# Kernel optimization log

Hardware: AMD Instinct MI355X
Metric: run time of the kernel (lower is better)

The kernel has to match this reference:

```python
import jax, jax.numpy as jnp
import numpy as np

H = 1024   # hidden_dim
NH = 16    # num_heads
HD = H // NH  # head_dim = 64
B, S = 2, 2048
LN_EPS = 1e-5


def setup_inputs() -> dict:
    key = jax.random.key(0)
    ks = jax.random.split(key, 5)
    scale = 1.0 / np.sqrt(H)  # xavier-ish scale for stability
    return {
        "x": jax.random.normal(ks[0], (B, S, H), dtype=jnp.float32),
        "Wq": jax.random.normal(ks[1], (H, H), dtype=jnp.float32) * scale,
        "bq": jnp.zeros((H,), jnp.float32),
        "Wk": jax.random.normal(ks[2], (H, H), dtype=jnp.float32) * scale,
        "bk": jnp.zeros((H,), jnp.float32),
        "Wv": jax.random.normal(ks[3], (H, H), dtype=jnp.float32) * scale,
        "bv": jnp.zeros((H,), jnp.float32),
        "Wo": jax.random.normal(ks[4], (H, H), dtype=jnp.float32) * scale,
        "bo": jnp.zeros((H,), jnp.float32),
        "ln_gamma": jnp.ones((H,), jnp.float32),
        "ln_beta": jnp.zeros((H,), jnp.float32),
    }


def reference(x, Wq, bq, Wk, bk, Wv, bv, Wo, bo, ln_gamma, ln_beta):
    b, s, _ = x.shape
    # QKV projections, split heads: (b, nh, s, hd)
    def split_heads(t):
        return t.reshape(b, s, NH, HD).transpose(0, 2, 1, 3)
    Q = split_heads(x @ Wq + bq)
    K = split_heads(x @ Wk + bk)
    V = split_heads(x @ Wv + bv)
    # scaled dot-product with clamp (mask=None path)
    scores = jnp.einsum('bhqd,bhkd->bhqk', Q, K) / np.sqrt(HD).astype(np.float32)
    scores = jnp.clip(scores, -10000.0, 10000.0)
    attn = jax.nn.softmax(scores, axis=-1)
    # dropout is identity in eval mode
    ctx = jnp.einsum('bhqk,bhkd->bhqd', attn, V)
    ctx = ctx.transpose(0, 2, 1, 3).reshape(b, s, H)
    out = ctx @ Wo + bo
    # residual + LayerNorm
    y = out + x
    mu = jnp.mean(y, axis=-1, keepdims=True)
    var = jnp.mean(jnp.square(y - mu), axis=-1, keepdims=True)
    y = (y - mu) * jax.lax.rsqrt(var + LN_EPS)
    return y * ln_gamma + ln_beta
```

## Files before the change

kernel.cpp:

```cpp
#include <hip/hip_runtime.h>

typedef unsigned short u16;
typedef __attribute__((ext_vector_type(8))) short shortx8;
typedef __attribute__((ext_vector_type(4))) float floatx4;
typedef __attribute__((ext_vector_type(2))) float floatx2;
typedef __attribute__((ext_vector_type(2))) unsigned uintx2;
typedef __attribute__((ext_vector_type(4))) unsigned uintx4;

#define GLD16(gp, lp) __builtin_amdgcn_global_load_lds( \
    (__attribute__((address_space(1))) void*)(gp), \
    (__attribute__((address_space(3))) void*)(lp), 16, 0, 0)

#define BAR() __builtin_amdgcn_s_barrier()
#define LGKM0() do { asm volatile("s_waitcnt lgkmcnt(0)" ::: "memory"); \
                     __builtin_amdgcn_sched_barrier(0); } while (0)
#define VMCNT0() do { asm volatile("s_waitcnt vmcnt(0)" ::: "memory"); \
                      __builtin_amdgcn_sched_barrier(0); } while (0)

__device__ __forceinline__ u16 f2bf(float f) {
  union { float f; unsigned u; } v; v.f = f;
  unsigned r = v.u + 0x7FFFu + ((v.u >> 16) & 1u);
  return (u16)(r >> 16);
}

__device__ __forceinline__ unsigned pkbf(float a, float b) {
#if __has_builtin(__builtin_amdgcn_cvt_pk_bf16_f32)
  auto r = __builtin_amdgcn_cvt_pk_bf16_f32(a, b);
  return __builtin_bit_cast(unsigned, r);
#else
  union { float f; unsigned u; } x, y; x.f = a; y.f = b;
  return __builtin_amdgcn_perm(y.u + 0x8000u, x.u + 0x8000u, 0x07060302u);
#endif
}

__global__ __launch_bounds__(256) void prep_kernel(const float* __restrict__ x,
                                                   u16* __restrict__ xb,
                                                   const float* __restrict__ Wq,
                                                   const float* __restrict__ Wk,
                                                   const float* __restrict__ Wv,
                                                   const float* __restrict__ Wo,
                                                   u16* __restrict__ Wt) {
  __shared__ u16 tile[32][33];
  int bid = blockIdx.x;
  int tid = threadIdx.x;
  if (bid < 4096) {
    int i = bid * 256 + tid;
    float4 v = ((const float4*)x)[i];
    uintx2 o;
    o.x = pkbf(v.x, v.y);
    o.y = pkbf(v.z, v.w);
    ((uintx2*)xb)[i] = o;
  } else {
    int block = bid - 4096;
    int mat = block >> 10;
    int rem = block & 1023;
    const float* W = (mat == 0) ? Wq : (mat == 1) ? Wk : (mat == 2) ? Wv : Wo;
    u16* dst = Wt + (size_t)mat * 1024 * 1024;
    int n0 = (rem & 31) * 32, k0 = (rem >> 5) * 32;
    int tx = tid & 31, ty = tid >> 5;
    for (int i = 0; i < 4; ++i)
      tile[ty + i * 8][tx] = f2bf(W[(size_t)(k0 + ty + i * 8) * 1024 + n0 + tx]);
    __syncthreads();
    for (int i = 0; i < 4; ++i)
      dst[(size_t)(n0 + ty + i * 8) * 1024 + k0 + tx] = tile[tx][ty + i * 8];
  }
}

template <int MIB>
__device__ __forceinline__ void qkv_lda(const u16* Ah, int lrow, int lcol,
                                        shortx8 (&afr)[2][2]) {
#pragma unroll
  for (int j = 0; j < 2; ++j) {
    int rm = (MIB + j) * 16 + lcol;
#pragma unroll
    for (int kk = 0; kk < 2; ++kk)
      afr[j][kk] = *(const shortx8*)&Ah[rm * 64 + (((kk * 4 + lrow) ^ (rm & 7)) * 8)];
  }
}

template <int MIB>
__device__ __forceinline__ void qkv_mfma(floatx4 (&acc)[8][4],
                                         const shortx8 (&afr)[2][2],
                                         const shortx8 (&bfr)[4][2]) {
#pragma unroll
  for (int kk = 0; kk < 2; ++kk)
#pragma unroll
    for (int j = 0; j < 2; ++j)
#pragma unroll
      for (int ni = 0; ni < 4; ++ni)
        acc[MIB + j][ni] = __builtin_amdgcn_mfma_f32_16x16x32_bf16(
            afr[j][kk], bfr[ni][kk], acc[MIB + j][ni], 0, 0, 0);
}

__global__ __launch_bounds__(512, 2) void qkv_gemm(const u16* __restrict__ xb,
                                                   const u16* __restrict__ Wt,
                                                   const float* __restrict__ bq,
                                                   const float* __restrict__ bk,
                                                   const float* __restrict__ bv,
                                                   u16* __restrict__ Qh,
                                                   u16* __restrict__ Kh,
                                                   u16* __restrict__ Vth) {
  __shared__ u16 lds[65536];
  const int tid = threadIdx.x;
  const int wave = tid >> 6, lane = tid & 63;
  const int lrow = lane >> 4, lcol = lane & 15;
  const int wm = wave >> 2, wn = wave & 3;
  const int m0 = blockIdx.x * 256;
  const int nt = blockIdx.y;
  const int mat = nt >> 2;
  const int n0 = (nt & 3) * 256;
  const u16* Ag = xb;
  const u16* Bg = Wt + (size_t)mat * 1048576;

  const u16* sa[2][2];
  const u16* sb[2][2];
#pragma unroll
  for (int h = 0; h < 2; ++h)
#pragma unroll
    for (int l = 0; l < 2; ++l) {
      int g = (l * 8 + wave) * 64 + lane;
      int r = g >> 3, c = g & 7;
      int cc = (c ^ (r & 7)) * 8;
      sa[h][l] = Ag + (size_t)(m0 + h * 128 + r) * 1024 + cc;
      sb[h][l] = Bg + (size_t)(n0 + h * 128 + r) * 1024 + cc;
    }

  floatx4 acc[8][4];
#pragma unroll
  for (int mi = 0; mi < 8; ++mi)
#pragma unroll
    for (int ni = 0; ni < 4; ++ni)
      acc[mi][ni] = (floatx4){0.f, 0.f, 0.f, 0.f};

#pragma unroll
  for (int h = 0; h < 2; ++h)
#pragma unroll
    for (int l = 0; l < 2; ++l) {
      GLD16(sa[h][l], lds + h * 8192 + (l * 8 + wave) * 512);
      GLD16(sb[h][l], lds + 16384 + h * 8192 + (l * 8 + wave) * 512);
    }
  VMCNT0();
  BAR();

#pragma unroll 2
  for (int t = 0; t < 16; ++t) {
    const int rb = t & 1, wb = rb ^ 1;
    const u16* Ah = lds + rb * 32768 + wm * 8192;
    const u16* Bh = lds + rb * 32768 + 16384 + (wn >> 1) * 8192;
    u16* Aw = lds + wb * 32768;
    u16* Bw = lds + wb * 32768 + 16384;

    if (t < 15) {
      int k64 = (t + 1) * 64;
#pragma unroll
      for (int l = 0; l < 2; ++l) {
        GLD16(sa[0][l] + k64, Aw + (l * 8 + wave) * 512);
        GLD16(sa[1][l] + k64, Aw + 8192 + (l * 8 + wave) * 512);
      }
    }
    shortx8 bfr[4][2];
#pragma unroll
    for (int ni = 0; ni < 4; ++ni) {
      int rn = (wn & 1) * 64 + ni * 16 + lcol;
#pragma unroll
      for (int kk = 0; kk < 2; ++kk)
        bfr[ni][kk] = *(const shortx8*)&Bh[rn * 64 + (((kk * 4 + lrow) ^ (rn & 7)) * 8)];
    }
    {
      shortx8 afr[2][2];
      qkv_lda<0>(Ah, lrow, lcol, afr);
      BAR();
      LGKM0();
      __builtin_amdgcn_s_setprio(1);
      qkv_mfma<0>(acc, afr, bfr);
      __builtin_amdgcn_s_setprio(0);
      BAR();
    }
    if (t < 15) {
      int k64 = (t + 1) * 64;
#pragma unroll
      for (int l = 0; l < 2; ++l) {
        GLD16(sb[0][l] + k64, Bw + (l * 8 + wave) * 512);
        GLD16(sb[1][l] + k64, Bw + 8192 + (l * 8 + wave) * 512);
      }
    }
    {
      shortx8 afr[2][2];
      qkv_lda<2>(Ah, lrow, lcol, afr);
      BAR();
      LGKM0();
      __builtin_amdgcn_s_setprio(1);
      qkv_mfma<2>(acc, afr, bfr);
      __builtin_amdgcn_s_setprio(0);
      BAR();
    }
    {
      shortx8 afr[2][2];
      qkv_lda<4>(Ah, lrow, lcol, afr);
      BAR();
      LGKM0();
      __builtin_amdgcn_s_setprio(1);
      qkv_mfma<4>(acc, afr, bfr);
      __builtin_amdgcn_s_setprio(0);
      BAR();
    }
    {
      shortx8 afr[2][2];
      qkv_lda<6>(Ah, lrow, lcol, afr);
      BAR();
      LGKM0();
      __builtin_amdgcn_s_setprio(1);
      qkv_mfma<6>(acc, afr, bfr);
      __builtin_amdgcn_s_setprio(0);
      VMCNT0();
      BAR();
    }
  }

  const float* bias = (mat == 0) ? bq : (mat == 1) ? bk : bv;
  const float qscale = 0.18033688011f;

  if (mat < 2) {
    u16* dst = (mat == 0) ? Qh : Kh;
    float sc = (mat == 0) ? qscale : 1.0f;
#pragma unroll
    for (int mi = 0; mi < 8; ++mi) {
      int mb = wm * 128 + mi * 16 + lrow * 4;
#pragma unroll
      for (int ni = 0; ni < 4; ++ni) {
        int n = wn * 64 + ni * 16 + lcol;
        float bval = bias[n0 + n];
#pragma unroll
        for (int r = 0; r < 4; ++r) {
          int m = mb + r;
          lds[m * 256 + (((n >> 3) ^ (m & 31)) * 8) + (n & 7)] =
              f2bf((acc[mi][ni][r] + bval) * sc);
        }
      }
    }
    __syncthreads();
    int row = tid >> 1, half = tid & 1;
    int m = m0 + row;
    int bb = m >> 11, s = m & 2047;
#pragma unroll
    for (int i = 0; i < 16; ++i) {
      int cg = half * 16 + i;
      int pg = cg ^ (row & 31);
      shortx8 v = *(const shortx8*)&lds[row * 256 + pg * 8];
      int ng = n0 + cg * 8;
      int hh = ng >> 6, d = ng & 63;
      *(shortx8*)&dst[((size_t)(bb * 16 + hh) * 2048 + s) * 64 + d] = v;
    }
  } else {
#pragma unroll
    for (int mi = 0; mi < 8; ++mi) {
      int mbase = m0 + wm * 128 + mi * 16 + lrow * 4;
      int bb = mbase >> 11, s = mbase & 2047;
#pragma unroll
      for (int ni = 0; ni < 4; ++ni) {
        int n = n0 + wn * 64 + ni * 16 + lcol;
        float bval = bias[n];
        int hh = n >> 6, d = n & 63;
        uintx2 pk;
        pk.x = pkbf(acc[mi][ni][0] + bval, acc[mi][ni][1] + bval);
        pk.y = pkbf(acc[mi][ni][2] + bval, acc[mi][ni][3] + bval);
        *(uintx2*)&Vth[((size_t)(bb * 16 + hh) * 64 + d) * 2048 + s] = pk;
      }
    }
  }
}

__global__ __launch_bounds__(256) void out_gemm(const u16* __restrict__ ctx,
                                                const u16* __restrict__ Wot,
                                                const float* __restrict__ bo,
                                                float* __restrict__ aout) {
  __shared__ u16 As[128 * 64];
  __shared__ u16 Bs[64 * 64];
  int m0 = blockIdx.x * 128;
  int n0 = blockIdx.y * 64;
  const int tid = threadIdx.x;
  const int wave = tid >> 6, lane = tid & 63;
  const int lrow = lane >> 4, lcol = lane & 15;
  const int wm = wave >> 1, wn = wave & 1;

  floatx4 acc[4][2];
  for (int mi = 0; mi < 4; ++mi)
    for (int ni = 0; ni < 2; ++ni)
      acc[mi][ni] = (floatx4){0.f, 0.f, 0.f, 0.f};

  const u16* ap[4];
  const u16* bp[2];
  for (int l = 0; l < 4; ++l) {
    int g = (l * 4 + wave) * 64 + lane;
    int r = g >> 3, c = g & 7;
    ap[l] = ctx + (size_t)(m0 + r) * 1024 + (c ^ (r & 7)) * 8;
  }
  for (int l = 0; l < 2; ++l) {
    int g = (l * 4 + wave) * 64 + lane;
    int r = g >> 3, c = g & 7;
    bp[l] = Wot + (size_t)(n0 + r) * 1024 + (c ^ (r & 7)) * 8;
  }

  for (int k0 = 0; k0 < 1024; k0 += 64) {
    __syncthreads();
    for (int l = 0; l < 4; ++l) { GLD16(ap[l], As + (l * 4 + wave) * 512); ap[l] += 64; }
    for (int l = 0; l < 2; ++l) { GLD16(bp[l], Bs + (l * 4 + wave) * 512); bp[l] += 64; }
    __syncthreads();
    for (int kk = 0; kk < 2; ++kk) {
      shortx8 af[4], bf[2];
      for (int mi = 0; mi < 4; ++mi) {
        int row = wm * 64 + mi * 16 + lcol;
        int gr = (kk * 4 + lrow) ^ (row & 7);
        af[mi] = *(const shortx8*)&As[row * 64 + gr * 8];
      }
      for (int ni = 0; ni < 2; ++ni) {
        int row = wn * 32 + ni * 16 + lcol;
        int gr = (kk * 4 + lrow) ^ (row & 7);
        bf[ni] = *(const shortx8*)&Bs[row * 64 + gr * 8];
      }
      for (int mi = 0; mi < 4; ++mi)
        for (int ni = 0; ni < 2; ++ni)
          acc[mi][ni] = __builtin_amdgcn_mfma_f32_16x16x32_bf16(af[mi], bf[ni], acc[mi][ni], 0, 0, 0);
    }
  }

  for (int mi = 0; mi < 4; ++mi) {
    int mbase = m0 + wm * 64 + mi * 16 + lrow * 4;
    for (int ni = 0; ni < 2; ++ni) {
      int n = n0 + wn * 32 + ni * 16 + lcol;
      float bval = bo[n];
      for (int r = 0; r < 4; ++r)
        aout[(size_t)(mbase + r) * 1024 + n] = acc[mi][ni][r] + bval;
    }
  }
}

__global__ __launch_bounds__(512) void attn_kernel(const u16* __restrict__ Qh,
                                                   const u16* __restrict__ Kh,
                                                   const u16* __restrict__ Vth,
                                                   u16* __restrict__ ctx) {
  __shared__ u16 QPs[128 * 64];
  __shared__ u16 Ks[2][64 * 64];
  __shared__ u16 Vs[2][64 * 64];

  int bh = blockIdx.x;
  int b = bh >> 4, h = bh & 15;
  int q0 = blockIdx.y * 128;
  int tid = threadIdx.x;
  int wave = tid >> 6, lane = tid & 63;
  int lrow = lane >> 4, lcol = lane & 15;

  const u16* Qg = Qh + ((size_t)bh * 2048 + q0) * 64;
  for (int l = 0; l < 2; ++l) {
    int g = (l * 8 + wave) * 64 + lane;
    int r = g >> 3, c = g & 7;
    GLD16(Qg + r * 64 + ((c ^ (r & 7)) * 8), QPs + (l * 8 + wave) * 512);
  }

  const u16* Kbase = Kh + (size_t)bh * 2048 * 64;
  const u16* Vbase = Vth + (size_t)bh * 64 * 2048;

  int g = wave * 64 + lane;
  int gr = g >> 3, gc = g & 7;
  int cc = (gc ^ (gr & 7)) * 8;
  const u16* kp = Kbase + (size_t)gr * 64 + cc;

  const u16* vp = Vbase + (size_t)gr * 2048 + gc * 8;
  int hh = gc >> 2, ct = gc & 3;
  int ua = 4 * (ct & 1) + (ct >> 1);
  int chunkA = hh * 4 + (ua >> 1);
  int offA = gr * 128 + ((chunkA ^ (gr & 7)) * 16) + (ua & 1) * 8;
  int offB = gr * 128 + (((chunkA + 1) ^ (gr & 7)) * 16) + (ua & 1) * 8;

  {
    float4 vreg = *(const float4*)vp;
    vp += 64;
    GLD16(kp, (u16*)Ks + wave * 512);
    kp += 4096;
    char* vb = (char*)Vs;
    *(floatx2*)(vb + offA) = (floatx2){vreg.x, vreg.y};
    *(floatx2*)(vb + offB) = (floatx2){vreg.z, vreg.w};
  }
  __syncthreads();

  shortx8 qf[2];
  for (int kk = 0; kk < 2; ++kk) {
    int row = wave * 16 + lcol;
    int grr = (kk * 4 + lrow) ^ (row & 7);
    qf[kk] = *(const shortx8*)&QPs[row * 64 + grr * 8];
  }

  const short one_bf = (short)0x3F80;
  const shortx8 ones8 = {one_bf, one_bf, one_bf, one_bf, one_bf, one_bf, one_bf, one_bf};

  floatx4 o[4];
  floatx4 lacc = (floatx4){0.f, 0.f, 0.f, 0.f};
  for (int dt = 0; dt < 4; ++dt) o[dt] = (floatx4){0.f, 0.f, 0.f, 0.f};

  for (int i = 0; i < 32; ++i) {
    int cur = i & 1;
    float4 vreg;
    if (i < 31) {
      vreg = *(const float4*)vp;
      vp += 64;
      GLD16(kp, (u16*)Ks + (cur ^ 1) * 4096 + wave * 512);
      kp += 4096;
    }

    floatx4 sc[4];
    for (int kt = 0; kt < 4; ++kt)
      sc[kt] = (floatx4){0.f, 0.f, 0.f, 0.f};
    __builtin_amdgcn_s_setprio(1);
    for (int kk = 0; kk < 2; ++kk) {
      for (int kt = 0; kt < 4; ++kt) {
        int row = kt * 16 + lcol;
        int grr = (kk * 4 + lrow) ^ (row & 7);
        shortx8 kf = *(const shortx8*)&Ks[cur][row * 64 + grr * 8];
        sc[kt] = __builtin_amdgcn_mfma_f32_16x16x32_bf16(kf, qf[kk], sc[kt], 0, 0, 0);
      }
    }
    __builtin_amdgcn_s_setprio(0);

    float p[4][4];
    for (int kt = 0; kt < 4; ++kt)
      for (int r = 0; r < 4; ++r)
        p[kt][r] = __builtin_amdgcn_exp2f(sc[kt][r]);
    shortx8 pf[2];
    for (int kk = 0; kk < 2; ++kk) {
      uintx4 w;
      w.x = pkbf(p[2 * kk][0], p[2 * kk][1]);
      w.y = pkbf(p[2 * kk][2], p[2 * kk][3]);
      w.z = pkbf(p[2 * kk + 1][0], p[2 * kk + 1][1]);
      w.w = pkbf(p[2 * kk + 1][2], p[2 * kk + 1][3]);
      pf[kk] = __builtin_bit_cast(shortx8, w);
    }

    if (i < 31) {
      char* vb = (char*)Vs + (cur ^ 1) * 8192;
      *(floatx2*)(vb + offA) = (floatx2){vreg.x, vreg.y};
      *(floatx2*)(vb + offB) = (floatx2){vreg.z, vreg.w};
    }

    __builtin_amdgcn_s_setprio(1);
    for (int kk = 0; kk < 2; ++kk) {
      lacc = __builtin_amdgcn_mfma_f32_16x16x32_bf16(ones8, pf[kk], lacc, 0, 0, 0);
      for (int dt = 0; dt < 4; ++dt) {
        int row = dt * 16 + lcol;
        int grr = (kk * 4 + lrow) ^ (row & 7);
        shortx8 vf = *(const shortx8*)&Vs[cur][row * 64 + grr * 8];
        o[dt] = __builtin_amdgcn_mfma_f32_16x16x32_bf16(vf, pf[kk], o[dt], 0, 0, 0);
      }
    }
    __builtin_amdgcn_s_setprio(0);
    __syncthreads();
  }

  {
    float inv = 1.0f / lacc[0];
    int s = q0 + wave * 16 + lcol;
    u16* dst = ctx + (size_t)(b * 2048 + s) * 1024 + h * 64 + lrow * 4;
    for (int dt = 0; dt < 4; ++dt) {
      uintx2 pk;
      pk.x = pkbf(o[dt][0] * inv, o[dt][1] * inv);
      pk.y = pkbf(o[dt][2] * inv, o[dt][3] * inv);
      *(uintx2*)(dst + dt * 16) = pk;
    }
  }
}

__global__ __launch_bounds__(256) void ln_kernel(const float* __restrict__ aout,
                                                 const float* __restrict__ x,
                                                 const float* __restrict__ gamma,
                                                 const float* __restrict__ beta,
                                                 float* __restrict__ out) {
  int row = blockIdx.x;
  int t = threadIdx.x;
  const float4* a4 = (const float4*)(aout + (size_t)row * 1024);
  const float4* x4 = (const float4*)(x + (size_t)row * 1024);
  float4 v = a4[t];
  float4 xv = x4[t];
  v.x += xv.x; v.y += xv.y; v.z += xv.z; v.w += xv.w;
  float s = v.x + v.y + v.z + v.w;
  float s2 = v.x * v.x + v.y * v.y + v.z * v.z + v.w * v.w;
  for (int off = 1; off < 64; off <<= 1) {
    s += __shfl_xor(s, off, 64);
    s2 += __shfl_xor(s2, off, 64);
  }
  __shared__ float red[8];
  int wave = t >> 6, lane = t & 63;
  if (lane == 0) { red[wave] = s; red[4 + wave] = s2; }
  __syncthreads();
  s = red[0] + red[1] + red[2] + red[3];
  s2 = red[4] + red[5] + red[6] + red[7];
  float mu = s * (1.0f / 1024.0f);
  float var = s2 * (1.0f / 1024.0f) - mu * mu;
  float rstd = rsqrtf(var + 1e-5f);
  float4 g = ((const float4*)gamma)[t];
  float4 be = ((const float4*)beta)[t];
  float4 y;
  y.x = (v.x - mu) * rstd * g.x + be.x;
  y.y = (v.y - mu) * rstd * g.y + be.y;
  y.z = (v.z - mu) * rstd * g.z + be.z;
  y.w = (v.w - mu) * rstd * g.w + be.w;
  ((float4*)(out + (size_t)row * 1024))[t] = y;
}

extern "C" void kernel_launch(void* const* d_in, const int* in_sizes, int n_in,
                              void* d_out, int out_size, void* d_ws, size_t ws_size,
                              hipStream_t stream) {
  const float* x     = (const float*)d_in[0];
  const float* Wq    = (const float*)d_in[1];
  const float* bq    = (const float*)d_in[2];
  const float* Wk    = (const float*)d_in[3];
  const float* bk    = (const float*)d_in[4];
  const float* Wv    = (const float*)d_in[5];
  const float* bv    = (const float*)d_in[6];
  const float* Wo    = (const float*)d_in[7];
  const float* bo    = (const float*)d_in[8];
  const float* gamma = (const float*)d_in[9];
  const float* beta  = (const float*)d_in[10];
  float* out = (float*)d_out;

  char* ws = (char*)d_ws;
  u16* xb   = (u16*)(ws);
  u16* Wt   = (u16*)(ws + ((size_t)8 << 20));
  u16* Qh   = (u16*)(ws + ((size_t)16 << 20));
  u16* Kh   = (u16*)(ws + ((size_t)24 << 20));
  u16* Vth  = (u16*)(ws + ((size_t)32 << 20));
  u16* ctx  = (u16*)(ws + ((size_t)40 << 20));
  float* aout = (float*)(ws + ((size_t)48 << 20));

  prep_kernel<<<8192, 256, 0, stream>>>(x, xb, Wq, Wk, Wv, Wo, Wt);
  qkv_gemm<<<dim3(16, 12), 512, 0, stream>>>(xb, Wt, bq, bk, bv, Qh, Kh, Vth);
  attn_kernel<<<dim3(32, 16), 512, 0, stream>>>(Qh, Kh, Vth, ctx);
  out_gemm<<<dim3(32, 16), 256, 0, stream>>>(ctx, Wt + (size_t)3 * 1024 * 1024, bo, aout);
  ln_kernel<<<4096, 256, 0, stream>>>(aout, x, gamma, beta, out);
}
```

Baseline: 193.6 us.

## Halve attention block to 4 waves, each handling two query sub-tiles

The attention kernel now runs 256 threads (4 waves) per block instead of 8, and each wave processes 32 query rows as two 16-row sub-tiles. Every K and V fragment read from LDS is reused for two MFMAs, which halves LDS read traffic per unit of compute. Each thread issues two global loads per tile, and the launch bounds ask for two blocks per CU. The cost is higher register pressure from the doubled accumulators and fewer waves per block to hide latency.

```diff
diff --git a/kernel.cpp b/kernel.cpp
--- a/kernel.cpp
+++ b/kernel.cpp
@@ -335,10 +335,10 @@
   }
 }
 
-__global__ __launch_bounds__(512) void attn_kernel(const u16* __restrict__ Qh,
-                                                   const u16* __restrict__ Kh,
-                                                   const u16* __restrict__ Vth,
-                                                   u16* __restrict__ ctx) {
+__global__ __launch_bounds__(256, 2) void attn_kernel(const u16* __restrict__ Qh,
+                                                      const u16* __restrict__ Kh,
+                                                      const u16* __restrict__ Vth,
+                                                      u16* __restrict__ ctx) {
   __shared__ u16 QPs[128 * 64];
   __shared__ u16 Ks[2][64 * 64];
   __shared__ u16 Vs[2][64 * 64];
@@ -351,118 +351,157 @@
   int lrow = lane >> 4, lcol = lane & 15;
 
   const u16* Qg = Qh + ((size_t)bh * 2048 + q0) * 64;
-  for (int l = 0; l < 2; ++l) {
-    int g = (l * 8 + wave) * 64 + lane;
+#pragma unroll
+  for (int l = 0; l < 4; ++l) {
+    int g = (l * 4 + wave) * 64 + lane;
     int r = g >> 3, c = g & 7;
-    GLD16(Qg + r * 64 + ((c ^ (r & 7)) * 8), QPs + (l * 8 + wave) * 512);
+    GLD16(Qg + r * 64 + ((c ^ (r & 7)) * 8), QPs + (l * 4 + wave) * 512);
   }
 
   const u16* Kbase = Kh + (size_t)bh * 2048 * 64;
   const u16* Vbase = Vth + (size_t)bh * 64 * 2048;
 
-  int g = wave * 64 + lane;
-  int gr = g >> 3, gc = g & 7;
-  int cc = (gc ^ (gr & 7)) * 8;
-  const u16* kp = Kbase + (size_t)gr * 64 + cc;
-
-  const u16* vp = Vbase + (size_t)gr * 2048 + gc * 8;
-  int hh = gc >> 2, ct = gc & 3;
-  int ua = 4 * (ct & 1) + (ct >> 1);
-  int chunkA = hh * 4 + (ua >> 1);
-  int offA = gr * 128 + ((chunkA ^ (gr & 7)) * 16) + (ua & 1) * 8;
-  int offB = gr * 128 + (((chunkA + 1) ^ (gr & 7)) * 16) + (ua & 1) * 8;
+  const u16* kp[2];
+  const u16* vp[2];
+  int offA[2], offB[2];
+#pragma unroll
+  for (int l = 0; l < 2; ++l) {
+    int g = (l * 4 + wave) * 64 + lane;
+    int gr = g >> 3, gc = g & 7;
+    kp[l] = Kbase + (size_t)gr * 64 + ((gc ^ (gr & 7)) * 8);
+    vp[l] = Vbase + (size_t)gr * 2048 + gc * 8;
+    int hh = gc >> 2, ct = gc & 3;
+    int ua = 4 * (ct & 1) + (ct >> 1);
+    int chunkA = hh * 4 + (ua >> 1);
+    offA[l] = gr * 128 + ((chunkA ^ (gr & 7)) * 16) + (ua & 1) * 8;
+    offB[l] = gr * 128 + (((chunkA + 1) ^ (gr & 7)) * 16) + (ua & 1) * 8;
+  }
 
   {
-    float4 vreg = *(const float4*)vp;
-    vp += 64;
-    GLD16(kp, (u16*)Ks + wave * 512);
-    kp += 4096;
+    float4 v0 = *(const float4*)vp[0];
+    float4 v1 = *(const float4*)vp[1];
+    vp[0] += 64; vp[1] += 64;
+    GLD16(kp[0], (u16*)Ks + wave * 512);
+    GLD16(kp[1], (u16*)Ks + (4 + wave) * 512);
+    kp[0] += 4096; kp[1] += 4096;
     char* vb = (char*)Vs;
-    *(floatx2*)(vb + offA) = (floatx2){vreg.x, vreg.y};
-    *(floatx2*)(vb + offB) = (floatx2){vreg.z, vreg.w};
+    *(floatx2*)(vb + offA[0]) = (floatx2){v0.x, v0.y};
+    *(floatx2*)(vb + offB[0]) = (floatx2){v0.z, v0.w};
+    *(floatx2*)(vb + offA[1]) = (floatx2){v1.x, v1.y};
+    *(floatx2*)(vb + offB[1]) = (floatx2){v1.z, v1.w};
   }
   __syncthreads();
 
-  shortx8 qf[2];
-  for (int kk = 0; kk < 2; ++kk) {
-    int row = wave * 16 + lcol;
-    int grr = (kk * 4 + lrow) ^ (row & 7);
-    qf[kk] = *(const shortx8*)&QPs[row * 64 + grr * 8];
-  }
+  shortx8 qf[2][2];
+#pragma unroll
+  for (int s = 0; s < 2; ++s)
+#pragma unroll
+    for (int kk = 0; kk < 2; ++kk) {
+      int row = wave * 32 + s * 16 + lcol;
+      int grr = (kk * 4 + lrow) ^ (row & 7);
+      qf[s][kk] = *(const shortx8*)&QPs[row * 64 + grr * 8];
+    }
 
   const short one_bf = (short)0x3F80;
   const shortx8 ones8 = {one_bf, one_bf, one_bf, one_bf, one_bf, one_bf, one_bf, one_bf};
 
-  floatx4 o[4];
-  floatx4 lacc = (floatx4){0.f, 0.f, 0.f, 0.f};
-  for (int dt = 0; dt < 4; ++dt) o[dt] = (floatx4){0.f, 0.f, 0.f, 0.f};
+  floatx4 o[2][4];
+  floatx4 lacc[2];
+#pragma unroll
+  for (int s = 0; s < 2; ++s) {
+    lacc[s] = (floatx4){0.f, 0.f, 0.f, 0.f};
+#pragma unroll
+    for (int dt = 0; dt < 4; ++dt) o[s][dt] = (floatx4){0.f, 0.f, 0.f, 0.f};
+  }
 
   for (int i = 0; i < 32; ++i) {
     int cur = i & 1;
-    float4 vreg;
+    float4 v0, v1;
     if (i < 31) {
-      vreg = *(const float4*)vp;
-      vp += 64;
-      GLD16(kp, (u16*)Ks + (cur ^ 1) * 4096 + wave * 512);
-      kp += 4096;
-    }
-
-    floatx4 sc[4];
-    for (int kt = 0; kt < 4; ++kt)
-      sc[kt] = (floatx4){0.f, 0.f, 0.f, 0.f};
+      v0 = *(const float4*)vp[0];
+      v1 = *(const float4*)vp[1];
+      vp[0] += 64; vp[1] += 64;
+      GLD16(kp[0], (u16*)Ks + (cur ^ 1) * 4096 + wave * 512);
+      GLD16(kp[1], (u16*)Ks + (cur ^ 1) * 4096 + (4 + wave) * 512);
+      kp[0] += 4096; kp[1] += 4096;
+    }
+
+    floatx4 sc[2][4];
+#pragma unroll
+    for (int s = 0; s < 2; ++s)
+#pragma unroll
+      for (int kt = 0; kt < 4; ++kt)
+        sc[s][kt] = (floatx4){0.f, 0.f, 0.f, 0.f};
     __builtin_amdgcn_s_setprio(1);
+#pragma unroll
     for (int kk = 0; kk < 2; ++kk) {
+#pragma unroll
       for (int kt = 0; kt < 4; ++kt) {
         int row = kt * 16 + lcol;
         int grr = (kk * 4 + lrow) ^ (row & 7);
         shortx8 kf = *(const shortx8*)&Ks[cur][row * 64 + grr * 8];
-        sc[kt] = __builtin_amdgcn_mfma_f32_16x16x32_bf16(kf, qf[kk], sc[kt], 0, 0, 0);
+        sc[0][kt] = __builtin_amdgcn_mfma_f32_16x16x32_bf16(kf, qf[0][kk], sc[0][kt], 0, 0, 0);
+        sc[1][kt] = __builtin_amdgcn_mfma_f32_16x16x32_bf16(kf, qf[1][kk], sc[1][kt], 0, 0, 0);
       }
     }
     __builtin_amdgcn_s_setprio(0);
 
-    float p[4][4];
-    for (int kt = 0; kt < 4; ++kt)
-      for (int r = 0; r < 4; ++r)
-        p[kt][r] = __builtin_amdgcn_exp2f(sc[kt][r]);
-    shortx8 pf[2];
-    for (int kk = 0; kk < 2; ++kk) {
-      uintx4 w;
-      w.x = pkbf(p[2 * kk][0], p[2 * kk][1]);
-      w.y = pkbf(p[2 * kk][2], p[2 * kk][3]);
-      w.z = pkbf(p[2 * kk + 1][0], p[2 * kk + 1][1]);
-      w.w = pkbf(p[2 * kk + 1][2], p[2 * kk + 1][3]);
-      pf[kk] = __builtin_bit_cast(shortx8, w);
+    shortx8 pf[2][2];
+#pragma unroll
+    for (int s = 0; s < 2; ++s) {
+      float p[4][4];
+#pragma unroll
+      for (int kt = 0; kt < 4; ++kt)
+#pragma unroll
+        for (int r = 0; r < 4; ++r)
+          p[kt][r] = __builtin_amdgcn_exp2f(sc[s][kt][r]);
+#pragma unroll
+      for (int kk = 0; kk < 2; ++kk) {
+        uintx4 w;
+        w.x = pkbf(p[2 * kk][0], p[2 * kk][1]);
+        w.y = pkbf(p[2 * kk][2], p[2 * kk][3]);
+        w.z = pkbf(p[2 * kk + 1][0], p[2 * kk + 1][1]);
+        w.w = pkbf(p[2 * kk + 1][2], p[2 * kk + 1][3]);
+        pf[s][kk] = __builtin_bit_cast(shortx8, w);
+      }
     }
 
     if (i < 31) {
       char* vb = (char*)Vs + (cur ^ 1) * 8192;
-      *(floatx2*)(vb + offA) = (floatx2){vreg.x, vreg.y};
-      *(floatx2*)(vb + offB) = (floatx2){vreg.z, vreg.w};
+      *(floatx2*)(vb + offA[0]) = (floatx2){v0.x, v0.y};
+      *(floatx2*)(vb + offB[0]) = (floatx2){v0.z, v0.w};
+      *(floatx2*)(vb + offA[1]) = (floatx2){v1.x, v1.y};
+      *(floatx2*)(vb + offB[1]) = (floatx2){v1.z, v1.w};
     }
 
     __builtin_amdgcn_s_setprio(1);
+#pragma unroll
     for (int kk = 0; kk < 2; ++kk) {
-      lacc = __builtin_amdgcn_mfma_f32_16x16x32_bf16(ones8, pf[kk], lacc, 0, 0, 0);
+      lacc[0] = __builtin_amdgcn_mfma_f32_16x16x32_bf16(ones8, pf[0][kk], lacc[0], 0, 0, 0);
+      lacc[1] = __builtin_amdgcn_mfma_f32_16x16x32_bf16(ones8, pf[1][kk], lacc[1], 0, 0, 0);
+#pragma unroll
       for (int dt = 0; dt < 4; ++dt) {
         int row = dt * 16 + lcol;
         int grr = (kk * 4 + lrow) ^ (row & 7);
         shortx8 vf = *(const shortx8*)&Vs[cur][row * 64 + grr * 8];
-        o[dt] = __builtin_amdgcn_mfma_f32_16x16x32_bf16(vf, pf[kk], o[dt], 0, 0, 0);
+        o[0][dt] = __builtin_amdgcn_mfma_f32_16x16x32_bf16(vf, pf[0][kk], o[0][dt], 0, 0, 0);
+        o[1][dt] = __builtin_amdgcn_mfma_f32_16x16x32_bf16(vf, pf[1][kk], o[1][dt], 0, 0, 0);
       }
     }
     __builtin_amdgcn_s_setprio(0);
     __syncthreads();
   }
 
-  {
-    float inv = 1.0f / lacc[0];
-    int s = q0 + wave * 16 + lcol;
-    u16* dst = ctx + (size_t)(b * 2048 + s) * 1024 + h * 64 + lrow * 4;
+#pragma unroll
+  for (int s = 0; s < 2; ++s) {
+    float inv = 1.0f / lacc[s][0];
+    int sq = q0 + wave * 32 + s * 16 + lcol;
+    u16* dst = ctx + (size_t)(b * 2048 + sq) * 1024 + h * 64 + lrow * 4;
+#pragma unroll
     for (int dt = 0; dt < 4; ++dt) {
       uintx2 pk;
-      pk.x = pkbf(o[dt][0] * inv, o[dt][1] * inv);
-      pk.y = pkbf(o[dt][2] * inv, o[dt][3] * inv);
+      pk.x = pkbf(o[s][dt][0] * inv, o[s][dt][1] * inv);
+      pk.y = pkbf(o[s][dt][2] * inv, o[s][dt][3] * inv);
       *(uintx2*)(dst + dt * 16) = pk;
     }
   }
@@ -532,7 +571,7 @@
 
   prep_kernel<<<8192, 256, 0, stream>>>(x, xb, Wq, Wk, Wv, Wo, Wt);
   qkv_gemm<<<dim3(16, 12), 512, 0, stream>>>(xb, Wt, bq, bk, bv, Qh, Kh, Vth);
-  attn_kernel<<<dim3(32, 16), 512, 0, stream>>>(Qh, Kh, Vth, ctx);
+  attn_kernel<<<dim3(32, 16), 256, 0, stream>>>(Qh, Kh, Vth, ctx);
   out_gemm<<<dim3(32, 16), 256, 0, stream>>>(ctx, Wt + (size_t)3 * 1024 * 1024, bo, aout);
   ln_kernel<<<4096, 256, 0, stream>>>(aout, x, gamma, beta, out);
 }
```

New measurement: 199.0 us. 1.03x slower.

## Double-buffer LDS in output projection GEMM with split-phase prefetch

Applied to the files above, without the earlier changes.

Rewrites the out_gemm main loop to use two LDS buffers. The next k-tile's A and B loads are issued asynchronously while MFMAs run on the current tile, with the work split into two half-phases under barriers and raised wave priority around the MFMA bursts. The aim is to hide global-to-LDS load latency that the old load/sync/compute loop exposed. In exchange it doubles LDS use and adds more barriers and a launch_bounds occupancy hint.

```diff
diff --git a/kernel.cpp b/kernel.cpp
--- a/kernel.cpp
+++ b/kernel.cpp
@@ -270,65 +270,129 @@
   }
 }
 
-__global__ __launch_bounds__(256) void out_gemm(const u16* __restrict__ ctx,
-                                                const u16* __restrict__ Wot,
-                                                const float* __restrict__ bo,
-                                                float* __restrict__ aout) {
-  __shared__ u16 As[128 * 64];
-  __shared__ u16 Bs[64 * 64];
-  int m0 = blockIdx.x * 128;
-  int n0 = blockIdx.y * 64;
+__global__ __launch_bounds__(256, 2) void out_gemm(const u16* __restrict__ ctx,
+                                                   const u16* __restrict__ Wot,
+                                                   const float* __restrict__ bo,
+                                                   float* __restrict__ aout) {
+  __shared__ u16 lds[24576];
   const int tid = threadIdx.x;
   const int wave = tid >> 6, lane = tid & 63;
   const int lrow = lane >> 4, lcol = lane & 15;
   const int wm = wave >> 1, wn = wave & 1;
-
-  floatx4 acc[4][2];
-  for (int mi = 0; mi < 4; ++mi)
-    for (int ni = 0; ni < 2; ++ni)
-      acc[mi][ni] = (floatx4){0.f, 0.f, 0.f, 0.f};
-
-  const u16* ap[4];
-  const u16* bp[2];
+  const int m0 = blockIdx.x * 128;
+  const int n0 = blockIdx.y * 64;
+
+  const u16* sa[4];
+  const u16* sb[2];
+#pragma unroll
   for (int l = 0; l < 4; ++l) {
     int g = (l * 4 + wave) * 64 + lane;
     int r = g >> 3, c = g & 7;
-    ap[l] = ctx + (size_t)(m0 + r) * 1024 + (c ^ (r & 7)) * 8;
-  }
+    sa[l] = ctx + (size_t)(m0 + r) * 1024 + ((c ^ (r & 7)) * 8);
+  }
+#pragma unroll
   for (int l = 0; l < 2; ++l) {
     int g = (l * 4 + wave) * 64 + lane;
     int r = g >> 3, c = g & 7;
-    bp[l] = Wot + (size_t)(n0 + r) * 1024 + (c ^ (r & 7)) * 8;
-  }
-
-  for (int k0 = 0; k0 < 1024; k0 += 64) {
-    __syncthreads();
-    for (int l = 0; l < 4; ++l) { GLD16(ap[l], As + (l * 4 + wave) * 512); ap[l] += 64; }
-    for (int l = 0; l < 2; ++l) { GLD16(bp[l], Bs + (l * 4 + wave) * 512); bp[l] += 64; }
-    __syncthreads();
-    for (int kk = 0; kk < 2; ++kk) {
-      shortx8 af[4], bf[2];
-      for (int mi = 0; mi < 4; ++mi) {
-        int row = wm * 64 + mi * 16 + lcol;
-        int gr = (kk * 4 + lrow) ^ (row & 7);
-        af[mi] = *(const shortx8*)&As[row * 64 + gr * 8];
-      }
-      for (int ni = 0; ni < 2; ++ni) {
-        int row = wn * 32 + ni * 16 + lcol;
-        int gr = (kk * 4 + lrow) ^ (row & 7);
-        bf[ni] = *(const shortx8*)&Bs[row * 64 + gr * 8];
-      }
-      for (int mi = 0; mi < 4; ++mi)
-        for (int ni = 0; ni < 2; ++ni)
-          acc[mi][ni] = __builtin_amdgcn_mfma_f32_16x16x32_bf16(af[mi], bf[ni], acc[mi][ni], 0, 0, 0);
-    }
-  }
-
+    sb[l] = Wot + (size_t)(n0 + r) * 1024 + ((c ^ (r & 7)) * 8);
+  }
+
+  floatx4 acc[4][2];
+#pragma unroll
+  for (int mi = 0; mi < 4; ++mi)
+#pragma unroll
+    for (int ni = 0; ni < 2; ++ni)
+      acc[mi][ni] = (floatx4){0.f, 0.f, 0.f, 0.f};
+
+#pragma unroll
+  for (int l = 0; l < 4; ++l) GLD16(sa[l], lds + (l * 4 + wave) * 512);
+#pragma unroll
+  for (int l = 0; l < 2; ++l) GLD16(sb[l], lds + 8192 + (l * 4 + wave) * 512);
+  VMCNT0();
+  BAR();
+
+#pragma unroll 2
+  for (int t = 0; t < 16; ++t) {
+    const int rb = t & 1, wb = rb ^ 1;
+    const u16* Ab = lds + rb * 12288;
+    const u16* Bb = lds + rb * 12288 + 8192;
+    u16* Aw = lds + wb * 12288;
+    u16* Bw = lds + wb * 12288 + 8192;
+    const int k64 = (t + 1) * 64;
+
+    if (t < 15) {
+#pragma unroll
+      for (int l = 0; l < 4; ++l) GLD16(sa[l] + k64, Aw + (l * 4 + wave) * 512);
+    }
+    shortx8 bfr[2][2];
+#pragma unroll
+    for (int ni = 0; ni < 2; ++ni) {
+      int rn = wn * 32 + ni * 16 + lcol;
+#pragma unroll
+      for (int kk = 0; kk < 2; ++kk)
+        bfr[ni][kk] = *(const shortx8*)&Bb[rn * 64 + (((kk * 4 + lrow) ^ (rn & 7)) * 8)];
+    }
+    {
+      shortx8 afr[2][2];
+#pragma unroll
+      for (int j = 0; j < 2; ++j) {
+        int rm = wm * 64 + j * 16 + lcol;
+#pragma unroll
+        for (int kk = 0; kk < 2; ++kk)
+          afr[j][kk] = *(const shortx8*)&Ab[rm * 64 + (((kk * 4 + lrow) ^ (rm & 7)) * 8)];
+      }
+      BAR();
+      LGKM0();
+      __builtin_amdgcn_s_setprio(1);
+#pragma unroll
+      for (int kk = 0; kk < 2; ++kk)
+#pragma unroll
+        for (int j = 0; j < 2; ++j)
+#pragma unroll
+          for (int ni = 0; ni < 2; ++ni)
+            acc[j][ni] = __builtin_amdgcn_mfma_f32_16x16x32_bf16(
+                afr[j][kk], bfr[ni][kk], acc[j][ni], 0, 0, 0);
+      __builtin_amdgcn_s_setprio(0);
+      BAR();
+    }
+    if (t < 15) {
+#pragma unroll
+      for (int l = 0; l < 2; ++l) GLD16(sb[l] + k64, Bw + (l * 4 + wave) * 512);
+    }
+    {
+      shortx8 afr[2][2];
+#pragma unroll
+      for (int j = 0; j < 2; ++j) {
+        int rm = wm * 64 + (2 + j) * 16 + lcol;
+#pragma unroll
+        for (int kk = 0; kk < 2; ++kk)
+          afr[j][kk] = *(const shortx8*)&Ab[rm * 64 + (((kk * 4 + lrow) ^ (rm & 7)) * 8)];
+      }
+      BAR();
+      LGKM0();
+      __builtin_amdgcn_s_setprio(1);
+#pragma unroll
+      for (int kk = 0; kk < 2; ++kk)
+#pragma unroll
+        for (int j = 0; j < 2; ++j)
+#pragma unroll
+          for (int ni = 0; ni < 2; ++ni)
+            acc[2 + j][ni] = __builtin_amdgcn_mfma_f32_16x16x32_bf16(
+                afr[j][kk], bfr[ni][kk], acc[2 + j][ni], 0, 0, 0);
+      __builtin_amdgcn_s_setprio(0);
+      VMCNT0();
+      BAR();
+    }
+  }
+
+#pragma unroll
   for (int mi = 0; mi < 4; ++mi) {
     int mbase = m0 + wm * 64 + mi * 16 + lrow * 4;
+#pragma unroll
     for (int ni = 0; ni < 2; ++ni) {
       int n = n0 + wn * 32 + ni * 16 + lcol;
       float bval = bo[n];
+#pragma unroll
       for (int r = 0; r < 4; ++r)
         aout[(size_t)(mbase + r) * 1024 + n] = acc[mi][ni][r] + bval;
     }
```

Result: no change. 193.0 us (-0.3%).

## Fuse output projection GEMM with residual add and LayerNorm

Applied to the files above, without the earlier changes.

Replaces the separate out_gemm and ln_kernel with one kernel. Each block computes a full 16-row by 1024-column output tile, then adds bias and residual, reduces mean and variance across waves in shared memory, and writes the normalized result. This removes the fp32 intermediate round trip to global memory and one launch. In exchange, only 256 blocks of 512 threads run, each with a skinny M=16 tile. The Wo operand is read straight from global memory into registers without LDS staging, so each block re-reads all of Wo and data reuse drops.

```diff
diff --git a/kernel.cpp b/kernel.cpp
--- a/kernel.cpp
+++ b/kernel.cpp
@@ -270,71 +270,6 @@
   }
 }
 
-__global__ __launch_bounds__(256) void out_gemm(const u16* __restrict__ ctx,
-                                                const u16* __restrict__ Wot,
-                                                const float* __restrict__ bo,
-                                                float* __restrict__ aout) {
-  __shared__ u16 As[128 * 64];
-  __shared__ u16 Bs[64 * 64];
-  int m0 = blockIdx.x * 128;
-  int n0 = blockIdx.y * 64;
-  const int tid = threadIdx.x;
-  const int wave = tid >> 6, lane = tid & 63;
-  const int lrow = lane >> 4, lcol = lane & 15;
-  const int wm = wave >> 1, wn = wave & 1;
-
-  floatx4 acc[4][2];
-  for (int mi = 0; mi < 4; ++mi)
-    for (int ni = 0; ni < 2; ++ni)
-      acc[mi][ni] = (floatx4){0.f, 0.f, 0.f, 0.f};
-
-  const u16* ap[4];
-  const u16* bp[2];
-  for (int l = 0; l < 4; ++l) {
-    int g = (l * 4 + wave) * 64 + lane;
-    int r = g >> 3, c = g & 7;
-    ap[l] = ctx + (size_t)(m0 + r) * 1024 + (c ^ (r & 7)) * 8;
-  }
-  for (int l = 0; l < 2; ++l) {
-    int g = (l * 4 + wave) * 64 + lane;
-    int r = g >> 3, c = g & 7;
-    bp[l] = Wot + (size_t)(n0 + r) * 1024 + (c ^ (r & 7)) * 8;
-  }
-
-  for (int k0 = 0; k0 < 1024; k0 += 64) {
-    __syncthreads();
-    for (int l = 0; l < 4; ++l) { GLD16(ap[l], As + (l * 4 + wave) * 512); ap[l] += 64; }
-    for (int l = 0; l < 2; ++l) { GLD16(bp[l], Bs + (l * 4 + wave) * 512); bp[l] += 64; }
-    __syncthreads();
-    for (int kk = 0; kk < 2; ++kk) {
-      shortx8 af[4], bf[2];
-      for (int mi = 0; mi < 4; ++mi) {
-        int row = wm * 64 + mi * 16 + lcol;
-        int gr = (kk * 4 + lrow) ^ (row & 7);
-        af[mi] = *(const shortx8*)&As[row * 64 + gr * 8];
-      }
-      for (int ni = 0; ni < 2; ++ni) {
-        int row = wn * 32 + ni * 16 + lcol;
-        int gr = (kk * 4 + lrow) ^ (row & 7);
-        bf[ni] = *(const shortx8*)&Bs[row * 64 + gr * 8];
-      }
-      for (int mi = 0; mi < 4; ++mi)
-        for (int ni = 0; ni < 2; ++ni)
-          acc[mi][ni] = __builtin_amdgcn_mfma_f32_16x16x32_bf16(af[mi], bf[ni], acc[mi][ni], 0, 0, 0);
-    }
-  }
-
-  for (int mi = 0; mi < 4; ++mi) {
-    int mbase = m0 + wm * 64 + mi * 16 + lrow * 4;
-    for (int ni = 0; ni < 2; ++ni) {
-      int n = n0 + wn * 32 + ni * 16 + lcol;
-      float bval = bo[n];
-      for (int r = 0; r < 4; ++r)
-        aout[(size_t)(mbase + r) * 1024 + n] = acc[mi][ni][r] + bval;
-    }
-  }
-}
-
 __global__ __launch_bounds__(512) void attn_kernel(const u16* __restrict__ Qh,
                                                    const u16* __restrict__ Kh,
                                                    const u16* __restrict__ Vth,
@@ -468,41 +403,113 @@
   }
 }
 
-__global__ __launch_bounds__(256) void ln_kernel(const float* __restrict__ aout,
+__global__ __launch_bounds__(512, 1) void out_ln(const u16* __restrict__ ctx,
+                                                 const u16* __restrict__ Wot,
+                                                 const float* __restrict__ bo,
                                                  const float* __restrict__ x,
                                                  const float* __restrict__ gamma,
                                                  const float* __restrict__ beta,
                                                  float* __restrict__ out) {
-  int row = blockIdx.x;
-  int t = threadIdx.x;
-  const float4* a4 = (const float4*)(aout + (size_t)row * 1024);
-  const float4* x4 = (const float4*)(x + (size_t)row * 1024);
-  float4 v = a4[t];
-  float4 xv = x4[t];
-  v.x += xv.x; v.y += xv.y; v.z += xv.z; v.w += xv.w;
-  float s = v.x + v.y + v.z + v.w;
-  float s2 = v.x * v.x + v.y * v.y + v.z * v.z + v.w * v.w;
-  for (int off = 1; off < 64; off <<= 1) {
-    s += __shfl_xor(s, off, 64);
-    s2 += __shfl_xor(s2, off, 64);
-  }
-  __shared__ float red[8];
-  int wave = t >> 6, lane = t & 63;
-  if (lane == 0) { red[wave] = s; red[4 + wave] = s2; }
+  __shared__ u16 As[16 * 1024];
+  __shared__ float redS[8][16];
+  __shared__ float redQ[8][16];
+  const int tid = threadIdx.x;
+  const int wave = tid >> 6, lane = tid & 63;
+  const int lrow = lane >> 4, lcol = lane & 15;
+  const int m0 = blockIdx.x * 16;
+
+#pragma unroll
+  for (int l = 0; l < 4; ++l) {
+    int j = (l * 8 + wave) * 64 + lane;
+    int t = j >> 7, rem = j & 127;
+    int row = rem >> 3, cc = rem & 7;
+    GLD16(ctx + (size_t)(m0 + row) * 1024 + t * 64 + ((cc ^ (row & 7)) * 8),
+          (u16*)As + (l * 8 + wave) * 512);
+  }
+  VMCNT0();
+  BAR();
+
+  const u16* bp[8];
+#pragma unroll
+  for (int ni = 0; ni < 8; ++ni) {
+    int n = wave * 128 + ni * 16 + lcol;
+    bp[ni] = Wot + (size_t)n * 1024 + lrow * 8;
+  }
+
+  floatx4 acc[8];
+#pragma unroll
+  for (int ni = 0; ni < 8; ++ni) acc[ni] = (floatx4){0.f, 0.f, 0.f, 0.f};
+
+#pragma unroll 1
+  for (int t = 0; t < 16; ++t) {
+    shortx8 bfr[8][2];
+#pragma unroll
+    for (int ni = 0; ni < 8; ++ni)
+#pragma unroll
+      for (int kk = 0; kk < 2; ++kk)
+        bfr[ni][kk] = *(const shortx8*)(bp[ni] + t * 64 + kk * 32);
+    shortx8 afr[2];
+#pragma unroll
+    for (int kk = 0; kk < 2; ++kk)
+      afr[kk] = *(const shortx8*)&As[t * 1024 + lcol * 64 +
+                                     (((kk * 4 + lrow) ^ (lcol & 7)) * 8)];
+#pragma unroll
+    for (int kk = 0; kk < 2; ++kk)
+#pragma unroll
+      for (int ni = 0; ni < 8; ++ni)
+        acc[ni] = __builtin_amdgcn_mfma_f32_16x16x32_bf16(afr[kk], bfr[ni][kk], acc[ni], 0, 0, 0);
+  }
+
+  float s1[4] = {0.f, 0.f, 0.f, 0.f};
+  float sq[4] = {0.f, 0.f, 0.f, 0.f};
+#pragma unroll
+  for (int ni = 0; ni < 8; ++ni) {
+    int n = wave * 128 + ni * 16 + lcol;
+    float bval = bo[n];
+#pragma unroll
+    for (int r = 0; r < 4; ++r) {
+      float v = acc[ni][r] + bval + x[(size_t)(m0 + lrow * 4 + r) * 1024 + n];
+      acc[ni][r] = v;
+      s1[r] += v;
+      sq[r] += v * v;
+    }
+  }
+#pragma unroll
+  for (int off = 1; off < 16; off <<= 1) {
+#pragma unroll
+    for (int r = 0; r < 4; ++r) {
+      s1[r] += __shfl_xor(s1[r], off, 64);
+      sq[r] += __shfl_xor(sq[r], off, 64);
+    }
+  }
+  if (lcol == 0) {
+#pragma unroll
+    for (int r = 0; r < 4; ++r) {
+      redS[wave][lrow * 4 + r] = s1[r];
+      redQ[wave][lrow * 4 + r] = sq[r];
+    }
+  }
   __syncthreads();
-  s = red[0] + red[1] + red[2] + red[3];
-  s2 = red[4] + red[5] + red[6] + red[7];
-  float mu = s * (1.0f / 1024.0f);
-  float var = s2 * (1.0f / 1024.0f) - mu * mu;
-  float rstd = rsqrtf(var + 1e-5f);
-  float4 g = ((const float4*)gamma)[t];
-  float4 be = ((const float4*)beta)[t];
-  float4 y;
-  y.x = (v.x - mu) * rstd * g.x + be.x;
-  y.y = (v.y - mu) * rstd * g.y + be.y;
-  y.z = (v.z - mu) * rstd * g.z + be.z;
-  y.w = (v.w - mu) * rstd * g.w + be.w;
-  ((float4*)(out + (size_t)row * 1024))[t] = y;
+  float mu[4], rs[4];
+#pragma unroll
+  for (int r = 0; r < 4; ++r) {
+    int row = lrow * 4 + r;
+    float ts = 0.f, tq = 0.f;
+#pragma unroll
+    for (int w = 0; w < 8; ++w) { ts += redS[w][row]; tq += redQ[w][row]; }
+    float m = ts * (1.0f / 1024.0f);
+    mu[r] = m;
+    rs[r] = rsqrtf(tq * (1.0f / 1024.0f) - m * m + 1e-5f);
+  }
+#pragma unroll
+  for (int ni = 0; ni < 8; ++ni) {
+    int n = wave * 128 + ni * 16 + lcol;
+    float gg = gamma[n];
+    float be = beta[n];
+#pragma unroll
+    for (int r = 0; r < 4; ++r)
+      out[(size_t)(m0 + lrow * 4 + r) * 1024 + n] = (acc[ni][r] - mu[r]) * rs[r] * gg + be;
+  }
 }
 
 extern "C" void kernel_launch(void* const* d_in, const int* in_sizes, int n_in,
@@ -528,11 +535,9 @@
   u16* Kh   = (u16*)(ws + ((size_t)24 << 20));
   u16* Vth  = (u16*)(ws + ((size_t)32 << 20));
   u16* ctx  = (u16*)(ws + ((size_t)40 << 20));
-  float* aout = (float*)(ws + ((size_t)48 << 20));
 
   prep_kernel<<<8192, 256, 0, stream>>>(x, xb, Wq, Wk, Wv, Wo, Wt);
   qkv_gemm<<<dim3(16, 12), 512, 0, stream>>>(xb, Wt, bq, bk, bv, Qh, Kh, Vth);
   attn_kernel<<<dim3(32, 16), 512, 0, stream>>>(Qh, Kh, Vth, ctx);
-  out_gemm<<<dim3(32, 16), 256, 0, stream>>>(ctx, Wt + (size_t)3 * 1024 * 1024, bo, aout);
-  ln_kernel<<<4096, 256, 0, stream>>>(aout, x, gamma, beta, out);
-}
+  out_ln<<<256, 512, 0, stream>>>(ctx, Wt + (size_t)3 * 1024 * 1024, bo, x, gamma, beta, out);
+}
```

New measurement: 232.7 us. 1.2x slower.
